# Performance work log

Measured on AMD Instinct MI355X. Metric: run time of the kernel, lower is better.

The kernel has to match this reference:

```python
import jax, jax.numpy as jnp
import numpy as np

L = 8      # number of history layers backsubstituted (history[2:] in the torch code)
D = 2048   # layer width


def setup_inputs() -> dict:
    key = jax.random.key(0)
    ks = jax.random.split(key, 8)
    lower = jax.random.normal(ks[6], (D,), dtype=jnp.float32)
    upper = lower + jax.random.uniform(ks[7], (D,), dtype=jnp.float32)  # ensure lower <= upper
    return {
        "A": jax.random.normal(ks[0], (D, D), dtype=jnp.float32) * 0.05,
        "b": jax.random.normal(ks[1], (D,), dtype=jnp.float32) * 0.05,
        "hist_Al": jax.random.normal(ks[2], (L, D, D), dtype=jnp.float32) * 0.05,
        "hist_Au": jax.random.normal(ks[3], (L, D, D), dtype=jnp.float32) * 0.05,
        "hist_bl": jax.random.normal(ks[4], (L, D), dtype=jnp.float32) * 0.05,
        "hist_bu": jax.random.normal(ks[5], (L, D), dtype=jnp.float32) * 0.05,
        "lower_in": lower,
        "upper_in": upper,
    }


def reference(A, b, hist_Al, hist_Au, hist_bl, hist_bu, lower_in, upper_in):
    # Affine layer sets Al = Au = A, bl = bu = b, then backsubstitutes
    # through the history in reverse order (torch loop: i = len-1 .. 2).
    def step(carry, dp):
        Al, Au, bl, bu = carry
        dAl, dAu, dbl, dbu = dp
        Al_pos = jnp.maximum(Al, 0.0)
        Al_neg = jnp.minimum(Al, 0.0)
        Au_pos = jnp.maximum(Au, 0.0)
        Au_neg = jnp.minimum(Au, 0.0)
        new_Al = Al_pos @ dAl + Al_neg @ dAu
        new_bl = Al_pos @ dbl + Al_neg @ dbu + bl
        new_Au = Au_pos @ dAu + Au_neg @ dAl
        new_bu = Au_pos @ dbu + Au_neg @ dbl + bu
        return (new_Al, new_Au, new_bl, new_bu), None

    init = (A, A, b, b)
    # reverse the history so scan walks from the last layer back to the first
    dps = (hist_Al[::-1], hist_Au[::-1], hist_bl[::-1], hist_bu[::-1])
    (Al, Au, bl, bu), _ = jax.lax.scan(step, init, dps)

    # final concretization against the input box (history[1] in the torch code)
    lower = jnp.maximum(Al, 0.0) @ lower_in + jnp.minimum(Al, 0.0) @ upper_in + bl
    upper = jnp.maximum(Au, 0.0) @ upper_in + jnp.minimum(Au, 0.0) @ lower_in + bu
    return lower, upper
```

## Files before the change

kernel.cpp:

```cpp
#include <hip/hip_runtime.h>
#include <cstdint>
#include <cstddef>

#define D 2048
#define L 8
#define KT 4096
#define BM 256
#define BN 128
#define BK 64
#define NT (KT / BK)
#define BUFSZ ((BM + BN) * BK)

typedef _Float16 f16;
typedef _Float16 f16x4 __attribute__((ext_vector_type(4)));
typedef _Float16 f16x8 __attribute__((ext_vector_type(8)));
typedef float f32x4 __attribute__((ext_vector_type(4)));

__device__ __forceinline__ void gload16(const void* g, void* l) {
  __builtin_amdgcn_global_load_lds(
      (const __attribute__((address_space(1))) void*)g,
      (__attribute__((address_space(3))) void*)l, 16, 0, 0);
}

__global__ __launch_bounds__(256) void k_init(
    const float* __restrict__ A, const float* __restrict__ b,
    const float* __restrict__ db1, const float* __restrict__ db2,
    f16* __restrict__ Ab, float* __restrict__ blbu, float* __restrict__ outacc) {
  const int m = blockIdx.x, tid = threadIdx.x;
  if (m < 2) {
    f32x4 z = {0.f, 0.f, 0.f, 0.f};
    *(f32x4*)(outacc + m * 2048 + tid * 8) = z;
    *(f32x4*)(outacc + m * 2048 + tid * 8 + 4) = z;
  }
  const int k = tid * 8;
  size_t i = (size_t)m * D + k;
  f32x4 a0 = *(const f32x4*)(A + i);
  f32x4 a1 = *(const f32x4*)(A + i + 4);
  f16x8 p, n;
  float cL = 0.f, cU = 0.f;
#pragma unroll
  for (int j = 0; j < 8; ++j) {
    float v = (j < 4) ? a0[j] : a1[j - 4];
    float pf = fmaxf(v, 0.f), nf = fminf(v, 0.f);
    p[j] = (f16)pf; n[j] = (f16)nf;
    float w1 = db1[k + j], w2 = db2[k + j];
    cL += pf * w1 + nf * w2;
    cU += pf * w2 + nf * w1;
  }
  size_t lo = (size_t)m * KT + k;
  size_t hi = (size_t)(D + m) * KT + k;
  *(f16x8*)(Ab + lo) = p;      *(f16x8*)(Ab + lo + D) = n;
  *(f16x8*)(Ab + hi) = n;      *(f16x8*)(Ab + hi + D) = p;

  __shared__ float redL[4], redU[4];
#pragma unroll
  for (int off = 32; off > 0; off >>= 1) {
    cL += __shfl_down(cL, off);
    cU += __shfl_down(cU, off);
  }
  const int wave = tid >> 6, lane = tid & 63;
  if (lane == 0) { redL[wave] = cL; redU[wave] = cU; }
  __syncthreads();
  if (tid == 0) {
    float bL = b[m] + redL[0] + redL[1] + redL[2] + redL[3];
    float bU = b[m] + redU[0] + redU[1] + redU[2] + redU[3];
    blbu[m] = bL; blbu[D + m] = bU;
  }
}

__device__ __forceinline__ void transpose_panel(
    const float* __restrict__ srcAl, const float* __restrict__ srcAu,
    f16* __restrict__ Bb, int blk512, int tid) {
  const int z = blk512 >> 9;
  const int rem = blk512 & 511;
  const float* src = z ? srcAu : srcAl;
  const int koff = z ? D : 0;
  const int nb = (rem & 31) * 64;
  const int kb = (rem >> 5) * 128;
  const int lane = tid & 63, w = tid >> 6;
  const int col = nb + lane;
  const int k0 = kb + w * 16;
  float v[16];
#pragma unroll
  for (int j = 0; j < 16; ++j)
    v[j] = src[(size_t)(k0 + j) * D + col];
  f16x8 h0, h1;
#pragma unroll
  for (int j = 0; j < 8; ++j) { h0[j] = (f16)v[j]; h1[j] = (f16)v[8 + j]; }
  f16* dst = Bb + (size_t)col * KT + koff + k0;
  *(f16x8*)dst = h0;
  *(f16x8*)(dst + 8) = h1;
}

__global__ __launch_bounds__(512) void k_prep(
    const float* __restrict__ srcAl, const float* __restrict__ srcAu,
    f16* __restrict__ Bb) {
  transpose_panel(srcAl, srcAu, Bb, blockIdx.x, threadIdx.x);
}

__global__ __launch_bounds__(512, 2) void k_gemm(
    const f16* __restrict__ A,
    const f16* __restrict__ BT,
    f16* __restrict__ BTn,
    const float* __restrict__ nAl, const float* __restrict__ nAu,
    const float* __restrict__ w1, const float* __restrict__ w2,
    float* __restrict__ bdst,
    f16* __restrict__ An) {
  __shared__ __align__(16) f16 lds[3 * BUFSZ];

  if (blockIdx.x >= 256) {
    transpose_panel(nAl, nAu, BTn, blockIdx.x - 256, threadIdx.x);
    return;
  }

  const int flat = blockIdx.x;
  const int xcd = flat & 7, idx = flat >> 3;
  const int by = (xcd >> 1) * 4 + (idx >> 3);
  const int bx = (xcd & 1) * 8 + (idx & 7);
  const int m0 = by * BM;
  const int n0 = bx * BN;

  const int tid = threadIdx.x;
  const int wave = tid >> 6, lane = tid & 63;
  const int wm = (wave & 3) * 64, wn = (wave >> 2) * 64;
  const int sub = lane >> 3;
  const int cg = ((lane & 7) ^ sub) * 8;
  const int lr = lane & 15, lq = lane >> 4;

  f32x4 acc[4][4];
#pragma unroll
  for (int m = 0; m < 4; ++m)
#pragma unroll
    for (int n = 0; n < 4; ++n)
      acc[m][n] = (f32x4){0.f, 0.f, 0.f, 0.f};

  auto stage = [&](int kt, int buf) {
    f16* bA = lds + buf * BUFSZ;
    f16* bB = bA + BM * BK;
    const size_t gk = (size_t)kt * BK;
#pragma unroll
    for (int i = 0; i < 4; ++i) {
      const int r = i * 8 + wave;
      gload16(A + (size_t)(m0 + r * 8 + sub) * KT + gk + cg, bA + r * 512);
    }
#pragma unroll
    for (int i = 0; i < 2; ++i) {
      const int r = i * 8 + wave;
      gload16(BT + (size_t)(n0 + r * 8 + sub) * KT + gk + cg, bB + r * 512);
    }
  };

  stage(0, 0);
  stage(1, 1);
  asm volatile("s_waitcnt vmcnt(6)" ::: "memory");
  __builtin_amdgcn_sched_barrier(0);
  __builtin_amdgcn_s_barrier();
  __builtin_amdgcn_sched_barrier(0);

  for (int t = 0; t < NT; ++t) {
    const f16* bA = lds + (t % 3) * BUFSZ;
    const f16* bB = bA + BM * BK;
    if (t + 2 < NT) stage(t + 2, (t + 2) % 3);
#pragma unroll
    for (int s = 0; s < 2; ++s) {
      const int ch = ((s * 4 + lq) ^ (lane & 7)) * 8;
      f16x8 af[4], bf[4];
#pragma unroll
      for (int m = 0; m < 4; ++m)
        af[m] = *(const f16x8*)(bA + (wm + m * 16 + lr) * BK + ch);
#pragma unroll
      for (int n = 0; n < 4; ++n)
        bf[n] = *(const f16x8*)(bB + (wn + n * 16 + lr) * BK + ch);
      __builtin_amdgcn_s_setprio(1);
#pragma unroll
      for (int m = 0; m < 4; ++m)
#pragma unroll
        for (int n = 0; n < 4; ++n)
          acc[m][n] = __builtin_amdgcn_mfma_f32_16x16x32_f16(
              bf[n], af[m], acc[m][n], 0, 0, 0);
      __builtin_amdgcn_s_setprio(0);
    }
    if (t + 2 < NT) {
      asm volatile("s_waitcnt vmcnt(6)" ::: "memory");
    } else if (t + 1 < NT) {
      asm volatile("s_waitcnt vmcnt(0)" ::: "memory");
    }
    __builtin_amdgcn_sched_barrier(0);
    __builtin_amdgcn_s_barrier();
    __builtin_amdgcn_sched_barrier(0);
  }

  const int low = (m0 < D) ? 1 : 0;
  f32x4 w1v[4], w2v[4];
#pragma unroll
  for (int n = 0; n < 4; ++n) {
    const int col = n0 + wn + n * 16 + lq * 4;
    w1v[n] = *(const f32x4*)(w1 + col);
    w2v[n] = *(const f32x4*)(w2 + col);
  }
  float rowsum[4] = {0.f, 0.f, 0.f, 0.f};
#pragma unroll
  for (int m = 0; m < 4; ++m) {
#pragma unroll
    for (int n = 0; n < 4; ++n) {
      const size_t row = (size_t)(m0 + wm + m * 16 + lr);
      const int col = n0 + wn + n * 16 + lq * 4;
      f16x4 p, q;
#pragma unroll
      for (int r = 0; r < 4; ++r) {
        float v = acc[m][n][r];
        float pf = fmaxf(v, 0.f), qf = fminf(v, 0.f);
        p[r] = (f16)pf;
        q[r] = (f16)qf;
        float wa = low ? w1v[n][r] : w2v[n][r];
        float wb = low ? w2v[n][r] : w1v[n][r];
        rowsum[m] += pf * wa + qf * wb;
      }
      f16* base = An + row * KT + col;
      if (low) { *(f16x4*)base = p; *(f16x4*)(base + D) = q; }
      else     { *(f16x4*)base = q; *(f16x4*)(base + D) = p; }
    }
  }
#pragma unroll
  for (int m = 0; m < 4; ++m) {
    float v = rowsum[m];
    v += __shfl_down(v, 32);
    v += __shfl_down(v, 16);
    if (lane < 16)
      atomicAdd(bdst + m0 + wm + m * 16 + lane, v);
  }
}

__global__ __launch_bounds__(256) void k_final(
    const float* __restrict__ outacc, const float* __restrict__ blbu,
    float* __restrict__ out) {
  const int R = blockIdx.x * 256 + threadIdx.x;
  out[R] = outacc[R] + blbu[R];
}

extern "C" void kernel_launch(void* const* d_in, const int* in_sizes, int n_in,
                              void* d_out, int out_size, void* d_ws, size_t ws_size,
                              hipStream_t stream) {
  (void)in_sizes; (void)n_in; (void)out_size;
  const float* A   = (const float*)d_in[0];
  const float* b   = (const float*)d_in[1];
  const float* hAl = (const float*)d_in[2];
  const float* hAu = (const float*)d_in[3];
  const float* hbl = (const float*)d_in[4];
  const float* hbu = (const float*)d_in[5];
  const float* lo  = (const float*)d_in[6];
  const float* up  = (const float*)d_in[7];
  float* out = (float*)d_out;

  const size_t AS = (size_t)2 * D * KT;
  const size_t BS = (size_t)D * KT;
  const size_t MS = (size_t)D * D;
  char* base = (char*)d_ws;
  f16* Ab0   = (f16*)base;
  f16* Ab1   = Ab0 + AS;
  f16* Bb0   = Ab1 + AS;
  float* blbu   = (float*)(Bb0 + BS);
  float* outacc = blbu + 2 * D;
  f16* Bb1   = (f16*)(outacc + 2 * D);
  const size_t need_fused = (size_t)((char*)(Bb1 + BS) - base);
  const bool fused = ws_size >= need_fused;

  k_init<<<dim3(D), 256, 0, stream>>>(
      A, b, hbl + (size_t)7 * D, hbu + (size_t)7 * D, Ab0, blbu, outacc);
  k_prep<<<dim3(1024), 512, 0, stream>>>(
      hAl + (size_t)7 * MS, hAu + (size_t)7 * MS, Bb0);

  f16* cur = Ab0;
  f16* nxt = Ab1;
  for (int t = 0; t < L; ++t) {
    const int nlayer = 6 - t;
    const float* w1 = (t < 7) ? hbl + (size_t)nlayer * D : lo;
    const float* w2 = (t < 7) ? hbu + (size_t)nlayer * D : up;
    float* bd = (t < 7) ? blbu : outacc;
    f16* BT  = (fused && (t & 1)) ? Bb1 : Bb0;
    f16* BTn = fused ? ((t & 1) ? Bb0 : Bb1) : Bb0;
    const float* nl = (t < 7) ? hAl + (size_t)nlayer * MS : hAl;
    const float* nu = (t < 7) ? hAu + (size_t)nlayer * MS : hAu;
    if (!fused && t > 0)
      k_prep<<<dim3(1024), 512, 0, stream>>>(
          hAl + (size_t)(7 - t) * MS, hAu + (size_t)(7 - t) * MS, Bb0);
    const unsigned grid = (fused && t < 7) ? 1280u : 256u;
    k_gemm<<<dim3(grid), 512, 0, stream>>>(cur, BT, BTn, nl, nu, w1, w2, bd, nxt);
    f16* tmp = cur; cur = nxt; nxt = tmp;
  }
  k_final<<<dim3(2 * D / 256), 256, 0, stream>>>(outacc, blbu, out);
}
```

Measured before the change: 695.0 us.

## Use 4-wave GEMM blocks with BK=32 and 128x64 per-wave tiles

Moves the GEMM from 8 waves of 64x64 tiles to 4 waves of 128x64 tiles per 256x128 block and halves the K step to 32. LDS per buffer shrinks and the XOR swizzle on LDS rows is dropped. The transpose panel work is split into twice as many 256-thread blocks to match. The aim is more MFMA work per LDS fragment load, plus room for more resident blocks. The costs are higher register pressure from 32 accumulators, possible LDS bank conflicts without the swizzle, and twice as many barriers per K.

Result: slower. 764.8 us (+10.0%).

```diff
diff --git a/kernel.cpp b/kernel.cpp
--- a/kernel.cpp
+++ b/kernel.cpp
@@ -7,7 +7,7 @@
 #define KT 4096
 #define BM 256
 #define BN 128
-#define BK 64
+#define BK 32
 #define NT (KT / BK)
 #define BUFSZ ((BM + BN) * BK)
 
@@ -70,16 +70,15 @@
 
 __device__ __forceinline__ void transpose_panel(
     const float* __restrict__ srcAl, const float* __restrict__ srcAu,
-    f16* __restrict__ Bb, int blk512, int tid) {
-  const int z = blk512 >> 9;
-  const int rem = blk512 & 511;
+    f16* __restrict__ Bb, int blk, int tid) {
+  const int z = blk >> 10;
+  const int rem = blk & 1023;
   const float* src = z ? srcAu : srcAl;
   const int koff = z ? D : 0;
   const int nb = (rem & 31) * 64;
-  const int kb = (rem >> 5) * 128;
-  const int lane = tid & 63, w = tid >> 6;
-  const int col = nb + lane;
-  const int k0 = kb + w * 16;
+  const int kb = (rem >> 5) * 64;
+  const int col = nb + (tid & 63);
+  const int k0 = kb + (tid >> 6) * 16;
   float v[16];
 #pragma unroll
   for (int j = 0; j < 16; ++j)
@@ -92,13 +91,13 @@
   *(f16x8*)(dst + 8) = h1;
 }
 
-__global__ __launch_bounds__(512) void k_prep(
+__global__ __launch_bounds__(256) void k_prep(
     const float* __restrict__ srcAl, const float* __restrict__ srcAu,
     f16* __restrict__ Bb) {
   transpose_panel(srcAl, srcAu, Bb, blockIdx.x, threadIdx.x);
 }
 
-__global__ __launch_bounds__(512, 2) void k_gemm(
+__global__ __launch_bounds__(256, 2) void k_gemm(
     const f16* __restrict__ A,
     const f16* __restrict__ BT,
     f16* __restrict__ BTn,
@@ -122,14 +121,14 @@
 
   const int tid = threadIdx.x;
   const int wave = tid >> 6, lane = tid & 63;
-  const int wm = (wave & 3) * 64, wn = (wave >> 2) * 64;
-  const int sub = lane >> 3;
-  const int cg = ((lane & 7) ^ sub) * 8;
+  const int wm = (wave >> 1) * 128, wn = (wave & 1) * 64;
   const int lr = lane & 15, lq = lane >> 4;
-
-  f32x4 acc[4][4];
-#pragma unroll
-  for (int m = 0; m < 4; ++m)
+  const int srow = lane >> 2;
+  const int scol = (lane & 3) * 8;
+
+  f32x4 acc[8][4];
+#pragma unroll
+  for (int m = 0; m < 8; ++m)
 #pragma unroll
     for (int n = 0; n < 4; ++n)
       acc[m][n] = (f32x4){0.f, 0.f, 0.f, 0.f};
@@ -140,13 +139,13 @@
     const size_t gk = (size_t)kt * BK;
 #pragma unroll
     for (int i = 0; i < 4; ++i) {
-      const int r = i * 8 + wave;
-      gload16(A + (size_t)(m0 + r * 8 + sub) * KT + gk + cg, bA + r * 512);
+      const int r = i * 4 + wave;
+      gload16(A + (size_t)(m0 + r * 16 + srow) * KT + gk + scol, bA + r * 512);
     }
 #pragma unroll
     for (int i = 0; i < 2; ++i) {
-      const int r = i * 8 + wave;
-      gload16(BT + (size_t)(n0 + r * 8 + sub) * KT + gk + cg, bB + r * 512);
+      const int r = i * 4 + wave;
+      gload16(BT + (size_t)(n0 + r * 16 + srow) * KT + gk + scol, bB + r * 512);
     }
   };
 
@@ -161,25 +160,21 @@
     const f16* bA = lds + (t % 3) * BUFSZ;
     const f16* bB = bA + BM * BK;
     if (t + 2 < NT) stage(t + 2, (t + 2) % 3);
-#pragma unroll
-    for (int s = 0; s < 2; ++s) {
-      const int ch = ((s * 4 + lq) ^ (lane & 7)) * 8;
-      f16x8 af[4], bf[4];
-#pragma unroll
-      for (int m = 0; m < 4; ++m)
-        af[m] = *(const f16x8*)(bA + (wm + m * 16 + lr) * BK + ch);
+    f16x8 af[8], bf[4];
+#pragma unroll
+    for (int m = 0; m < 8; ++m)
+      af[m] = *(const f16x8*)(bA + (wm + m * 16 + lr) * BK + lq * 8);
+#pragma unroll
+    for (int n = 0; n < 4; ++n)
+      bf[n] = *(const f16x8*)(bB + (wn + n * 16 + lr) * BK + lq * 8);
+    __builtin_amdgcn_s_setprio(1);
+#pragma unroll
+    for (int m = 0; m < 8; ++m)
 #pragma unroll
       for (int n = 0; n < 4; ++n)
-        bf[n] = *(const f16x8*)(bB + (wn + n * 16 + lr) * BK + ch);
-      __builtin_amdgcn_s_setprio(1);
-#pragma unroll
-      for (int m = 0; m < 4; ++m)
-#pragma unroll
-        for (int n = 0; n < 4; ++n)
-          acc[m][n] = __builtin_amdgcn_mfma_f32_16x16x32_f16(
-              bf[n], af[m], acc[m][n], 0, 0, 0);
-      __builtin_amdgcn_s_setprio(0);
-    }
+        acc[m][n] = __builtin_amdgcn_mfma_f32_16x16x32_f16(
+            bf[n], af[m], acc[m][n], 0, 0, 0);
+    __builtin_amdgcn_s_setprio(0);
     if (t + 2 < NT) {
       asm volatile("s_waitcnt vmcnt(6)" ::: "memory");
     } else if (t + 1 < NT) {
@@ -198,9 +193,9 @@
     w1v[n] = *(const f32x4*)(w1 + col);
     w2v[n] = *(const f32x4*)(w2 + col);
   }
-  float rowsum[4] = {0.f, 0.f, 0.f, 0.f};
-#pragma unroll
-  for (int m = 0; m < 4; ++m) {
+  float rowsum[8] = {0.f, 0.f, 0.f, 0.f, 0.f, 0.f, 0.f, 0.f};
+#pragma unroll
+  for (int m = 0; m < 8; ++m) {
 #pragma unroll
     for (int n = 0; n < 4; ++n) {
       const size_t row = (size_t)(m0 + wm + m * 16 + lr);
@@ -222,7 +217,7 @@
     }
   }
 #pragma unroll
-  for (int m = 0; m < 4; ++m) {
+  for (int m = 0; m < 8; ++m) {
     float v = rowsum[m];
     v += __shfl_down(v, 32);
     v += __shfl_down(v, 16);
@@ -267,7 +262,7 @@
 
   k_init<<<dim3(D), 256, 0, stream>>>(
       A, b, hbl + (size_t)7 * D, hbu + (size_t)7 * D, Ab0, blbu, outacc);
-  k_prep<<<dim3(1024), 512, 0, stream>>>(
+  k_prep<<<dim3(2048), 256, 0, stream>>>(
       hAl + (size_t)7 * MS, hAu + (size_t)7 * MS, Bb0);
 
   f16* cur = Ab0;
@@ -282,10 +277,10 @@
     const float* nl = (t < 7) ? hAl + (size_t)nlayer * MS : hAl;
     const float* nu = (t < 7) ? hAu + (size_t)nlayer * MS : hAu;
     if (!fused && t > 0)
-      k_prep<<<dim3(1024), 512, 0, stream>>>(
+      k_prep<<<dim3(2048), 256, 0, stream>>>(
           hAl + (size_t)(7 - t) * MS, hAu + (size_t)(7 - t) * MS, Bb0);
-    const unsigned grid = (fused && t < 7) ? 1280u : 256u;
-    k_gemm<<<dim3(grid), 512, 0, stream>>>(cur, BT, BTn, nl, nu, w1, w2, bd, nxt);
+    const unsigned grid = (fused && t < 7) ? 2304u : 256u;
+    k_gemm<<<dim3(grid), 256, 0, stream>>>(cur, BT, BTn, nl, nu, w1, w2, bd, nxt);
     f16* tmp = cur; cur = nxt; nxt = tmp;
   }
   k_final<<<dim3(2 * D / 256), 256, 0, stream>>>(outacc, blbu, out);
```

## Interleave next-layer transpose into GEMM main loop instead of extra blocks

Applied to the files above, without the earlier changes.

The GEMM kernel used to append 1024 extra blocks that transposed and converted the next history layer to fp16. Now each of the 256 GEMM blocks does eight small transpose chunks inside its K loop, issuing global loads at one step and storing them two steps later, with the vmcnt wait relaxed to allow for them. The aim is to hide the transpose traffic behind MFMA work and avoid the tail of separate blocks. A wstate flag also skips writing the split An state on the last layer, since nothing reads it. The cost is higher register pressure and extra memory traffic inside the main loop, which could disturb the tuned pipeline.

New measurement: 661.0 us. -4.9%, faster.

```diff
diff --git a/kernel.cpp b/kernel.cpp
--- a/kernel.cpp
+++ b/kernel.cpp
@@ -70,26 +70,21 @@
 
 __device__ __forceinline__ void transpose_panel(
     const float* __restrict__ srcAl, const float* __restrict__ srcAu,
-    f16* __restrict__ Bb, int blk512, int tid) {
-  const int z = blk512 >> 9;
-  const int rem = blk512 & 511;
+    f16* __restrict__ Bb, int p, int tid) {
+  const int z = p >> 10;
+  const int rem = p & 1023;
   const float* src = z ? srcAu : srcAl;
   const int koff = z ? D : 0;
-  const int nb = (rem & 31) * 64;
-  const int kb = (rem >> 5) * 128;
-  const int lane = tid & 63, w = tid >> 6;
-  const int col = nb + lane;
-  const int k0 = kb + w * 16;
-  float v[16];
-#pragma unroll
-  for (int j = 0; j < 16; ++j)
+  const int col = (rem & 31) * 64 + (tid & 63);
+  const int k0 = (rem >> 5) * 64 + (tid >> 6) * 8;
+  float v[8];
+#pragma unroll
+  for (int j = 0; j < 8; ++j)
     v[j] = src[(size_t)(k0 + j) * D + col];
-  f16x8 h0, h1;
-#pragma unroll
-  for (int j = 0; j < 8; ++j) { h0[j] = (f16)v[j]; h1[j] = (f16)v[8 + j]; }
-  f16* dst = Bb + (size_t)col * KT + koff + k0;
-  *(f16x8*)dst = h0;
-  *(f16x8*)(dst + 8) = h1;
+  f16x8 h;
+#pragma unroll
+  for (int j = 0; j < 8; ++j) h[j] = (f16)v[j];
+  *(f16x8*)(Bb + (size_t)col * KT + koff + k0) = h;
 }
 
 __global__ __launch_bounds__(512) void k_prep(
@@ -105,13 +100,9 @@
     const float* __restrict__ nAl, const float* __restrict__ nAu,
     const float* __restrict__ w1, const float* __restrict__ w2,
     float* __restrict__ bdst,
-    f16* __restrict__ An) {
+    f16* __restrict__ An,
+    const int do_tr, const int wstate) {
   __shared__ __align__(16) f16 lds[3 * BUFSZ];
-
-  if (blockIdx.x >= 256) {
-    transpose_panel(nAl, nAu, BTn, blockIdx.x - 256, threadIdx.x);
-    return;
-  }
 
   const int flat = blockIdx.x;
   const int xcd = flat & 7, idx = flat >> 3;
@@ -157,9 +148,36 @@
   __builtin_amdgcn_s_barrier();
   __builtin_amdgcn_sched_barrier(0);
 
+  float trv[8];
+
   for (int t = 0; t < NT; ++t) {
     const f16* bA = lds + (t % 3) * BUFSZ;
     const f16* bB = bA + BM * BK;
+    const int tmod = t & 7;
+
+    if (do_tr && tmod == 4) {
+      const int p = (flat << 3) | ((t - 4) >> 3);
+      const int z = p >> 10, rem = p & 1023;
+      const int koff = z ? D : 0;
+      const int col = (rem & 31) * 64 + (tid & 63);
+      const int k0 = (rem >> 5) * 64 + (tid >> 6) * 8;
+      f16x8 h;
+#pragma unroll
+      for (int j = 0; j < 8; ++j) h[j] = (f16)trv[j];
+      *(f16x8*)(BTn + (size_t)col * KT + koff + k0) = h;
+    }
+    if (do_tr && tmod == 2) {
+      const int p = (flat << 3) | ((t - 2) >> 3);
+      const int z = p >> 10, rem = p & 1023;
+      const float* src = z ? nAu : nAl;
+      const int col = (rem & 31) * 64 + (tid & 63);
+      const int k0 = (rem >> 5) * 64 + (tid >> 6) * 8;
+#pragma unroll
+      for (int j = 0; j < 8; ++j)
+        trv[j] = src[(size_t)(k0 + j) * D + col];
+    }
+    __builtin_amdgcn_sched_barrier(0);
+
     if (t + 2 < NT) stage(t + 2, (t + 2) % 3);
 #pragma unroll
     for (int s = 0; s < 2; ++s) {
@@ -181,7 +199,11 @@
       __builtin_amdgcn_s_setprio(0);
     }
     if (t + 2 < NT) {
-      asm volatile("s_waitcnt vmcnt(6)" ::: "memory");
+      if (do_tr && tmod == 2) {
+        asm volatile("s_waitcnt vmcnt(14)" ::: "memory");
+      } else {
+        asm volatile("s_waitcnt vmcnt(6)" ::: "memory");
+      }
     } else if (t + 1 < NT) {
       asm volatile("s_waitcnt vmcnt(0)" ::: "memory");
     }
@@ -209,16 +231,18 @@
 #pragma unroll
       for (int r = 0; r < 4; ++r) {
         float v = acc[m][n][r];
-        float pf = fmaxf(v, 0.f), qf = fminf(v, 0.f);
-        p[r] = (f16)pf;
+        float pf2 = fmaxf(v, 0.f), qf = fminf(v, 0.f);
+        p[r] = (f16)pf2;
         q[r] = (f16)qf;
         float wa = low ? w1v[n][r] : w2v[n][r];
         float wb = low ? w2v[n][r] : w1v[n][r];
-        rowsum[m] += pf * wa + qf * wb;
+        rowsum[m] += pf2 * wa + qf * wb;
       }
-      f16* base = An + row * KT + col;
-      if (low) { *(f16x4*)base = p; *(f16x4*)(base + D) = q; }
-      else     { *(f16x4*)base = q; *(f16x4*)(base + D) = p; }
+      if (wstate) {
+        f16* base = An + row * KT + col;
+        if (low) { *(f16x4*)base = p; *(f16x4*)(base + D) = q; }
+        else     { *(f16x4*)base = q; *(f16x4*)(base + D) = p; }
+      }
     }
   }
 #pragma unroll
@@ -267,7 +291,7 @@
 
   k_init<<<dim3(D), 256, 0, stream>>>(
       A, b, hbl + (size_t)7 * D, hbu + (size_t)7 * D, Ab0, blbu, outacc);
-  k_prep<<<dim3(1024), 512, 0, stream>>>(
+  k_prep<<<dim3(2048), 512, 0, stream>>>(
       hAl + (size_t)7 * MS, hAu + (size_t)7 * MS, Bb0);
 
   f16* cur = Ab0;
@@ -282,10 +306,12 @@
     const float* nl = (t < 7) ? hAl + (size_t)nlayer * MS : hAl;
     const float* nu = (t < 7) ? hAu + (size_t)nlayer * MS : hAu;
     if (!fused && t > 0)
-      k_prep<<<dim3(1024), 512, 0, stream>>>(
+      k_prep<<<dim3(2048), 512, 0, stream>>>(
           hAl + (size_t)(7 - t) * MS, hAu + (size_t)(7 - t) * MS, Bb0);
-    const unsigned grid = (fused && t < 7) ? 1280u : 256u;
-    k_gemm<<<dim3(grid), 512, 0, stream>>>(cur, BT, BTn, nl, nu, w1, w2, bd, nxt);
+    const int do_tr = (fused && t < 7) ? 1 : 0;
+    const int wstate = (t < 7) ? 1 : 0;
+    k_gemm<<<dim3(256), 512, 0, stream>>>(cur, BT, BTn, nl, nu, w1, w2, bd,
+                                          nxt, do_tr, wstate);
     f16* tmp = cur; cur = nxt; nxt = tmp;
   }
   k_final<<<dim3(2 * D / 256), 256, 0, stream>>>(outacc, blbu, out);
```

## Rewrite backsubstitution via sum/difference matrices to halve stored state width

Applied to the files above, without the earlier changes.

The split into positive and negative parts is replaced by an identity: pos@dAl + neg@dAu equals A@(dAl+dAu)/2 + |A|@(dAl-dAu)/2, with the sign flipped on |A| for the upper rows. The state is now stored once in f16 with K=2048 instead of a [pos|neg] K=4096 layout. The |A| operand is built in registers by masking the f16 sign bit. The next layer's sum/difference transpose moves from extra blocks into the GEMM main loop, the pipeline becomes 4 stages with BK=32, and the final layer skips writing state. The MFMA count stays the same, so the saving comes from less state read/write traffic and fewer launched blocks. In exchange, the loop gains register pressure and extra interleaved global loads.

Result: faster. 670.5 us (-3.5%).

```diff
diff --git a/kernel.cpp b/kernel.cpp
--- a/kernel.cpp
+++ b/kernel.cpp
@@ -4,17 +4,18 @@
 
 #define D 2048
 #define L 8
-#define KT 4096
+#define KS 2048
 #define BM 256
-#define BN 128
-#define BK 64
-#define NT (KT / BK)
-#define BUFSZ ((BM + BN) * BK)
+#define BNR 256
+#define BK 32
+#define NT (KS / BK)
+#define BUFSZ ((BM + BNR) * BK)
 
 typedef _Float16 f16;
 typedef _Float16 f16x4 __attribute__((ext_vector_type(4)));
 typedef _Float16 f16x8 __attribute__((ext_vector_type(8)));
 typedef float f32x4 __attribute__((ext_vector_type(4)));
+typedef unsigned int u32x4 __attribute__((ext_vector_type(4)));
 
 __device__ __forceinline__ void gload16(const void* g, void* l) {
   __builtin_amdgcn_global_load_lds(
@@ -36,21 +37,19 @@
   size_t i = (size_t)m * D + k;
   f32x4 a0 = *(const f32x4*)(A + i);
   f32x4 a1 = *(const f32x4*)(A + i + 4);
-  f16x8 p, n;
+  f16x8 h;
   float cL = 0.f, cU = 0.f;
 #pragma unroll
   for (int j = 0; j < 8; ++j) {
     float v = (j < 4) ? a0[j] : a1[j - 4];
+    h[j] = (f16)v;
     float pf = fmaxf(v, 0.f), nf = fminf(v, 0.f);
-    p[j] = (f16)pf; n[j] = (f16)nf;
     float w1 = db1[k + j], w2 = db2[k + j];
     cL += pf * w1 + nf * w2;
     cU += pf * w2 + nf * w1;
   }
-  size_t lo = (size_t)m * KT + k;
-  size_t hi = (size_t)(D + m) * KT + k;
-  *(f16x8*)(Ab + lo) = p;      *(f16x8*)(Ab + lo + D) = n;
-  *(f16x8*)(Ab + hi) = n;      *(f16x8*)(Ab + hi + D) = p;
+  *(f16x8*)(Ab + (size_t)m * KS + k) = h;
+  *(f16x8*)(Ab + (size_t)(D + m) * KS + k) = h;
 
   __shared__ float redL[4], redU[4];
 #pragma unroll
@@ -68,64 +67,61 @@
   }
 }
 
-__device__ __forceinline__ void transpose_panel(
-    const float* __restrict__ srcAl, const float* __restrict__ srcAu,
-    f16* __restrict__ Bb, int blk512, int tid) {
-  const int z = blk512 >> 9;
-  const int rem = blk512 & 511;
-  const float* src = z ? srcAu : srcAl;
-  const int koff = z ? D : 0;
-  const int nb = (rem & 31) * 64;
-  const int kb = (rem >> 5) * 128;
-  const int lane = tid & 63, w = tid >> 6;
-  const int col = nb + lane;
-  const int k0 = kb + w * 16;
-  float v[16];
-#pragma unroll
-  for (int j = 0; j < 16; ++j)
-    v[j] = src[(size_t)(k0 + j) * D + col];
-  f16x8 h0, h1;
-#pragma unroll
-  for (int j = 0; j < 8; ++j) { h0[j] = (f16)v[j]; h1[j] = (f16)v[8 + j]; }
-  f16* dst = Bb + (size_t)col * KT + koff + k0;
-  *(f16x8*)dst = h0;
-  *(f16x8*)(dst + 8) = h1;
-}
-
 __global__ __launch_bounds__(512) void k_prep(
     const float* __restrict__ srcAl, const float* __restrict__ srcAu,
     f16* __restrict__ Bb) {
-  transpose_panel(srcAl, srcAu, Bb, blockIdx.x, threadIdx.x);
+  const int p = blockIdx.x, tid = threadIdx.x;
+  const size_t MS = (size_t)D * D;
+  const int col = (p & 31) * 64 + (tid & 63);
+  const int k0 = (p >> 5) * 64 + (tid >> 6) * 8;
+  float sl[8], su[8];
+#pragma unroll
+  for (int j = 0; j < 8; ++j) {
+    sl[j] = srcAl[(size_t)(k0 + j) * D + col];
+    su[j] = srcAu[(size_t)(k0 + j) * D + col];
+  }
+  f16x8 hs, hd;
+#pragma unroll
+  for (int j = 0; j < 8; ++j) {
+    hs[j] = (f16)((sl[j] + su[j]) * 0.5f);
+    hd[j] = (f16)((sl[j] - su[j]) * 0.5f);
+  }
+  *(f16x8*)(Bb + (size_t)col * KS + k0) = hs;
+  *(f16x8*)(Bb + MS + (size_t)col * KS + k0) = hd;
 }
 
 __global__ __launch_bounds__(512, 2) void k_gemm(
     const f16* __restrict__ A,
-    const f16* __restrict__ BT,
+    const f16* __restrict__ Bb,
     f16* __restrict__ BTn,
     const float* __restrict__ nAl, const float* __restrict__ nAu,
     const float* __restrict__ w1, const float* __restrict__ w2,
     float* __restrict__ bdst,
-    f16* __restrict__ An) {
-  __shared__ __align__(16) f16 lds[3 * BUFSZ];
-
-  if (blockIdx.x >= 256) {
-    transpose_panel(nAl, nAu, BTn, blockIdx.x - 256, threadIdx.x);
-    return;
-  }
+    f16* __restrict__ An,
+    const int do_tr, const int wstate) {
+  __shared__ __align__(16) f16 lds[4 * BUFSZ];
+  const size_t MS = (size_t)D * D;
 
   const int flat = blockIdx.x;
   const int xcd = flat & 7, idx = flat >> 3;
   const int by = (xcd >> 1) * 4 + (idx >> 3);
   const int bx = (xcd & 1) * 8 + (idx & 7);
   const int m0 = by * BM;
-  const int n0 = bx * BN;
+  const int n0 = bx * 128;
 
   const int tid = threadIdx.x;
   const int wave = tid >> 6, lane = tid & 63;
   const int wm = (wave & 3) * 64, wn = (wave >> 2) * 64;
-  const int sub = lane >> 3;
-  const int cg = ((lane & 7) ^ sub) * 8;
   const int lr = lane & 15, lq = lane >> 4;
+  const int srow = lane >> 2;
+  const int scol = ((lane & 3) ^ ((lane >> 3) & 3)) * 8;
+  const int rchunk = (lq ^ ((lr >> 1) & 3)) * 8;
+  const int low = (m0 < D) ? 1 : 0;
+  const unsigned amask = low ? 0x7FFF7FFFu : 0xFFFFFFFFu;
+  const unsigned omask = low ? 0x00000000u : 0x80008000u;
+
+  const f16* Bs = Bb;
+  const f16* Bd = Bb + MS;
 
   f32x4 acc[4][4];
 #pragma unroll
@@ -138,50 +134,93 @@
     f16* bA = lds + buf * BUFSZ;
     f16* bB = bA + BM * BK;
     const size_t gk = (size_t)kt * BK;
-#pragma unroll
-    for (int i = 0; i < 4; ++i) {
-      const int r = i * 8 + wave;
-      gload16(A + (size_t)(m0 + r * 8 + sub) * KT + gk + cg, bA + r * 512);
-    }
-#pragma unroll
-    for (int i = 0; i < 2; ++i) {
-      const int r = i * 8 + wave;
-      gload16(BT + (size_t)(n0 + r * 8 + sub) * KT + gk + cg, bB + r * 512);
-    }
+    gload16(A + (size_t)(m0 + wave * 16 + srow) * KS + gk + scol,
+            bA + wave * 512);
+    gload16(A + (size_t)(m0 + (wave + 8) * 16 + srow) * KS + gk + scol,
+            bA + (wave + 8) * 512);
+    gload16(Bs + (size_t)(n0 + wave * 16 + srow) * KS + gk + scol,
+            bB + wave * 512);
+    gload16(Bd + (size_t)(n0 + wave * 16 + srow) * KS + gk + scol,
+            bB + (wave + 8) * 512);
   };
 
-  stage(0, 0);
-  stage(1, 1);
-  asm volatile("s_waitcnt vmcnt(6)" ::: "memory");
+  stage(0, 0); stage(1, 1); stage(2, 2);
+  asm volatile("s_waitcnt vmcnt(8)" ::: "memory");
   __builtin_amdgcn_sched_barrier(0);
   __builtin_amdgcn_s_barrier();
   __builtin_amdgcn_sched_barrier(0);
 
+  float trl[8], tru[8];
+
   for (int t = 0; t < NT; ++t) {
-    const f16* bA = lds + (t % 3) * BUFSZ;
+    const f16* bA = lds + (t & 3) * BUFSZ;
     const f16* bB = bA + BM * BK;
-    if (t + 2 < NT) stage(t + 2, (t + 2) % 3);
-#pragma unroll
-    for (int s = 0; s < 2; ++s) {
-      const int ch = ((s * 4 + lq) ^ (lane & 7)) * 8;
-      f16x8 af[4], bf[4];
-#pragma unroll
-      for (int m = 0; m < 4; ++m)
-        af[m] = *(const f16x8*)(bA + (wm + m * 16 + lr) * BK + ch);
+    const int tmod = t & 15;
+
+    if (do_tr && tmod == 6) {
+      const int p = flat * 4 + ((t - 6) >> 4);
+      const int col = (p & 31) * 64 + (tid & 63);
+      const int k0 = (p >> 5) * 64 + (tid >> 6) * 8;
+      f16x8 hs, hd;
+#pragma unroll
+      for (int j = 0; j < 8; ++j) {
+        hs[j] = (f16)((trl[j] + tru[j]) * 0.5f);
+        hd[j] = (f16)((trl[j] - tru[j]) * 0.5f);
+      }
+      *(f16x8*)(BTn + (size_t)col * KS + k0) = hs;
+      *(f16x8*)(BTn + MS + (size_t)col * KS + k0) = hd;
+    }
+    if (do_tr && tmod == 2) {
+      const int p = flat * 4 + ((t - 2) >> 4);
+      const int col = (p & 31) * 64 + (tid & 63);
+      const int k0 = (p >> 5) * 64 + (tid >> 6) * 8;
+#pragma unroll
+      for (int j = 0; j < 8; ++j) {
+        trl[j] = nAl[(size_t)(k0 + j) * D + col];
+        tru[j] = nAu[(size_t)(k0 + j) * D + col];
+      }
+    }
+    __builtin_amdgcn_sched_barrier(0);
+
+    if (t + 3 < NT) stage(t + 3, (t + 3) & 3);
+
+    f16x8 a[4], bs4[4], bd4[4], ax[4];
+#pragma unroll
+    for (int m = 0; m < 4; ++m)
+      a[m] = *(const f16x8*)(bA + (wm + m * 16 + lr) * BK + rchunk);
+#pragma unroll
+    for (int n = 0; n < 4; ++n)
+      bs4[n] = *(const f16x8*)(bB + (wn + n * 16 + lr) * BK + rchunk);
+#pragma unroll
+    for (int n = 0; n < 4; ++n)
+      bd4[n] = *(const f16x8*)(bB + (128 + wn + n * 16 + lr) * BK + rchunk);
+#pragma unroll
+    for (int m = 0; m < 4; ++m) {
+      u32x4 u = *(const u32x4*)&a[m];
+      u = (u & amask) | omask;
+      ax[m] = *(const f16x8*)&u;
+    }
+    __builtin_amdgcn_s_setprio(1);
+#pragma unroll
+    for (int m = 0; m < 4; ++m)
 #pragma unroll
       for (int n = 0; n < 4; ++n)
-        bf[n] = *(const f16x8*)(bB + (wn + n * 16 + lr) * BK + ch);
-      __builtin_amdgcn_s_setprio(1);
-#pragma unroll
-      for (int m = 0; m < 4; ++m)
-#pragma unroll
-        for (int n = 0; n < 4; ++n)
-          acc[m][n] = __builtin_amdgcn_mfma_f32_16x16x32_f16(
-              bf[n], af[m], acc[m][n], 0, 0, 0);
-      __builtin_amdgcn_s_setprio(0);
-    }
-    if (t + 2 < NT) {
-      asm volatile("s_waitcnt vmcnt(6)" ::: "memory");
+        acc[m][n] = __builtin_amdgcn_mfma_f32_16x16x32_f16(
+            bs4[n], a[m], acc[m][n], 0, 0, 0);
+#pragma unroll
+    for (int m = 0; m < 4; ++m)
+#pragma unroll
+      for (int n = 0; n < 4; ++n)
+        acc[m][n] = __builtin_amdgcn_mfma_f32_16x16x32_f16(
+            bd4[n], ax[m], acc[m][n], 0, 0, 0);
+    __builtin_amdgcn_s_setprio(0);
+
+    if (t + 3 < NT) {
+      if (do_tr && (tmod == 2 || tmod == 3)) {
+        asm volatile("s_waitcnt vmcnt(24)" ::: "memory");
+      } else {
+        asm volatile("s_waitcnt vmcnt(8)" ::: "memory");
+      }
     } else if (t + 1 < NT) {
       asm volatile("s_waitcnt vmcnt(0)" ::: "memory");
     }
@@ -190,7 +229,6 @@
     __builtin_amdgcn_sched_barrier(0);
   }
 
-  const int low = (m0 < D) ? 1 : 0;
   f32x4 w1v[4], w2v[4];
 #pragma unroll
   for (int n = 0; n < 4; ++n) {
@@ -205,20 +243,18 @@
     for (int n = 0; n < 4; ++n) {
       const size_t row = (size_t)(m0 + wm + m * 16 + lr);
       const int col = n0 + wn + n * 16 + lq * 4;
-      f16x4 p, q;
+      f16x4 h;
 #pragma unroll
       for (int r = 0; r < 4; ++r) {
         float v = acc[m][n][r];
         float pf = fmaxf(v, 0.f), qf = fminf(v, 0.f);
-        p[r] = (f16)pf;
-        q[r] = (f16)qf;
+        h[r] = (f16)v;
         float wa = low ? w1v[n][r] : w2v[n][r];
         float wb = low ? w2v[n][r] : w1v[n][r];
         rowsum[m] += pf * wa + qf * wb;
       }
-      f16* base = An + row * KT + col;
-      if (low) { *(f16x4*)base = p; *(f16x4*)(base + D) = q; }
-      else     { *(f16x4*)base = q; *(f16x4*)(base + D) = p; }
+      if (wstate)
+        *(f16x4*)(An + row * KS + col) = h;
     }
   }
 #pragma unroll
@@ -252,8 +288,8 @@
   const float* up  = (const float*)d_in[7];
   float* out = (float*)d_out;
 
-  const size_t AS = (size_t)2 * D * KT;
-  const size_t BS = (size_t)D * KT;
+  const size_t AS = (size_t)2 * D * KS;
+  const size_t BS = (size_t)2 * D * D;
   const size_t MS = (size_t)D * D;
   char* base = (char*)d_ws;
   f16* Ab0   = (f16*)base;
@@ -284,8 +320,10 @@
     if (!fused && t > 0)
       k_prep<<<dim3(1024), 512, 0, stream>>>(
           hAl + (size_t)(7 - t) * MS, hAu + (size_t)(7 - t) * MS, Bb0);
-    const unsigned grid = (fused && t < 7) ? 1280u : 256u;
-    k_gemm<<<dim3(grid), 512, 0, stream>>>(cur, BT, BTn, nl, nu, w1, w2, bd, nxt);
+    const int do_tr = (fused && t < 7) ? 1 : 0;
+    const int wstate = (t < 7) ? 1 : 0;
+    k_gemm<<<dim3(256), 512, 0, stream>>>(cur, BT, BTn, nl, nu, w1, w2, bd,
+                                          nxt, do_tr, wstate);
     f16* tmp = cur; cur = nxt; nxt = tmp;
   }
   k_final<<<dim3(2 * D / 256), 256, 0, stream>>>(outacc, blbu, out);
```
